# Kernel optimization log

Hardware: AMD Instinct MI355X
Metric: run time of the kernel (lower is better)

The kernel has to match this reference:

```python
import jax, jax.numpy as jnp
import numpy as np

N = 4096      # nodes
IN = 512      # in_features
H = 8         # heads
D = 64        # out_features // heads (out % heads == 0)
EDGE_PROB = 0.01


def setup_inputs() -> dict:
    key = jax.random.key(0)
    kx, ka, kw, ko, kd = jax.random.split(key, 5)
    x = jax.random.normal(kx, (N, IN), dtype=jnp.float32)
    # dense binary adjacency with self-loops (original indexes adj[loc, :] as a mask)
    adj = (jax.random.uniform(ka, (N, N)) < EDGE_PROB).astype(jnp.float32)
    adj = jnp.maximum(adj, jnp.eye(N, dtype=jnp.float32))
    # stacked per-head params (original keeps Python lists of equal-sized heads)
    W = jax.random.normal(kw, (H, IN, D), dtype=jnp.float32) * (1.0 / np.sqrt(IN))
    a_origin = jax.random.normal(ko, (H, D), dtype=jnp.float32) * 0.1
    a_dst = jax.random.normal(kd, (H, D), dtype=jnp.float32) * 0.1
    return {"x": x, "adj": adj, "W": W, "a_origin": a_origin, "a_dst": a_dst}


def reference(x, adj, W, a_origin, a_dst):
    # per-head projection: mx[h] = x @ W[h]  -> [H, N, D]
    mx = jnp.einsum('nf,hfd->hnd', x, W)
    # clacAttn: e_ij = exp(mx_i . a_origin + mx_j . a_dst), masked by adj[i,:], row-normalised
    s_i = jnp.einsum('hnd,hd->hn', mx, a_origin)   # source term (row)
    t_j = jnp.einsum('hnd,hd->hn', mx, a_dst)      # dest term (col)
    logits = s_i[:, :, None] + t_j[:, None, :]     # [H, N, N]
    neg_inf = jnp.finfo(logits.dtype).min
    masked = jnp.where(adj[None] > 0, logits, neg_inf)
    attn = jax.nn.softmax(masked, axis=-1)         # == exp/masked-sum of original
    out_h = jnp.einsum('hij,hjd->hid', attn, mx)   # [H, N, D]
    # hstack over heads -> [N, H*D]
    return jnp.transpose(out_h, (1, 0, 2)).reshape(N, H * D)
```

## Files before the change

### kernel.cpp

```cpp
#include <hip/hip_runtime.h>
#include <hip/hip_bf16.h>

#define N_NODES 4096
#define IN_F    512
#define HEADS   8
#define DH      64
#define HD      512

typedef __bf16 bf16x8 __attribute__((ext_vector_type(8)));
typedef float  f32x4  __attribute__((ext_vector_type(4)));

__device__ __forceinline__ float bf_lo(unsigned u) { return __uint_as_float(u << 16); }
__device__ __forceinline__ float bf_hi(unsigned u) { return __uint_as_float(u & 0xffff0000u); }

#define MAXNBR 512
#define JCAP   128
__global__ __launch_bounds__(256) void k2_scan(const float* __restrict__ adj,
                                               int* __restrict__ deg,
                                               int* __restrict__ jl) {
    __shared__ int jlist[MAXNBR];
    __shared__ int cnt;
    int tid = threadIdx.x;
    int i   = blockIdx.x;
    int lane = tid & 63;
    if (tid == 0) cnt = 0;

    const uint4* arow = (const uint4*)(adj + (size_t)i * N_NODES);
    uint4 v0 = arow[tid];
    uint4 v1 = arow[256 + tid];
    uint4 v2 = arow[512 + tid];
    uint4 v3 = arow[768 + tid];
    int n = (v0.x != 0) + (v0.y != 0) + (v0.z != 0) + (v0.w != 0)
          + (v1.x != 0) + (v1.y != 0) + (v1.z != 0) + (v1.w != 0)
          + (v2.x != 0) + (v2.y != 0) + (v2.z != 0) + (v2.w != 0)
          + (v3.x != 0) + (v3.y != 0) + (v3.z != 0) + (v3.w != 0);
    __syncthreads();

    int pre = n;
    #pragma unroll
    for (int dlt = 1; dlt < 64; dlt <<= 1) {
        int t = __shfl_up(pre, dlt, 64);
        if (lane >= dlt) pre += t;
    }
    int wtot = __shfl(pre, 63, 64);
    int base = 0;
    if (lane == 63) base = atomicAdd(&cnt, wtot);
    base = __shfl(base, 63, 64);
    if (base + wtot <= MAXNBR) {
        int p_ = base + pre - n;
        int jb = tid * 4;
        if (v0.x) jlist[p_++] = jb;
        if (v0.y) jlist[p_++] = jb + 1;
        if (v0.z) jlist[p_++] = jb + 2;
        if (v0.w) jlist[p_++] = jb + 3;
        jb += 1024;
        if (v1.x) jlist[p_++] = jb;
        if (v1.y) jlist[p_++] = jb + 1;
        if (v1.z) jlist[p_++] = jb + 2;
        if (v1.w) jlist[p_++] = jb + 3;
        jb += 1024;
        if (v2.x) jlist[p_++] = jb;
        if (v2.y) jlist[p_++] = jb + 1;
        if (v2.z) jlist[p_++] = jb + 2;
        if (v2.w) jlist[p_++] = jb + 3;
        jb += 1024;
        if (v3.x) jlist[p_++] = jb;
        if (v3.y) jlist[p_++] = jb + 1;
        if (v3.z) jlist[p_++] = jb + 2;
        if (v3.w) jlist[p_++] = jb + 3;
    }
    __syncthreads();
    int c = cnt;
    if (c > JCAP) c = JCAP;
    for (int t = tid; t < c; t += 256) jl[(size_t)i * JCAP + t] = jlist[t];
    if (tid == 0) deg[i] = c;
}

#define KP 72

__global__ __launch_bounds__(256, 2) void k1_gemm(const float* __restrict__ X,
                                                  const float* __restrict__ W,
                                                  const float* __restrict__ a_dst,
                                                  __bf16* __restrict__ C,
                                                  float* __restrict__ et) {
    __shared__ __bf16 As[2][64][KP];
    __shared__ __bf16 Bs[2][64][KP];
    __shared__ float  ts[2][64];
    int tid  = threadIdx.x;
    int h    = blockIdx.x & 7;
    int y    = blockIdx.x >> 3;
    int row0 = y * 64, col0 = h * 64;
    int wave = tid >> 6, lane = tid & 63;
    int wm = wave >> 1, wn = wave & 1;
    int lr = lane & 15, kg = lane >> 4;

    f32x4 acc[2][2] = {};

    int sr = tid >> 3, sc = (tid & 7) * 8;
    const float* aptr0 = X + (size_t)(row0 + sr) * IN_F + sc;
    const float* aptr1 = aptr0 + (size_t)32 * IN_F;
    int dcol = tid & 63, fq = (tid >> 6) * 16;
    const float* wptr = W + ((size_t)h * IN_F + fq) * DH + dcol;

    f32x4 pa00 = *(const f32x4*)aptr0, pa01 = *(const f32x4*)(aptr0 + 4);
    f32x4 pa10 = *(const f32x4*)aptr1, pa11 = *(const f32x4*)(aptr1 + 4);
    float wv[16];
    #pragma unroll
    for (int i = 0; i < 16; ++i) wv[i] = wptr[(size_t)i * DH];

    float ad0 = a_dst[h * DH + wn * 32 + lr];
    float ad1 = a_dst[h * DH + wn * 32 + 16 + lr];

    #pragma unroll
    for (int k = 0; k < IN_F / 64; ++k) {
        int cur = k & 1;
        bf16x8 a0 = { (__bf16)pa00[0], (__bf16)pa00[1], (__bf16)pa00[2], (__bf16)pa00[3],
                      (__bf16)pa01[0], (__bf16)pa01[1], (__bf16)pa01[2], (__bf16)pa01[3] };
        bf16x8 a1 = { (__bf16)pa10[0], (__bf16)pa10[1], (__bf16)pa10[2], (__bf16)pa10[3],
                      (__bf16)pa11[0], (__bf16)pa11[1], (__bf16)pa11[2], (__bf16)pa11[3] };
        bf16x8 b0 = { (__bf16)wv[0],  (__bf16)wv[1],  (__bf16)wv[2],  (__bf16)wv[3],
                      (__bf16)wv[4],  (__bf16)wv[5],  (__bf16)wv[6],  (__bf16)wv[7] };
        bf16x8 b1 = { (__bf16)wv[8],  (__bf16)wv[9],  (__bf16)wv[10], (__bf16)wv[11],
                      (__bf16)wv[12], (__bf16)wv[13], (__bf16)wv[14], (__bf16)wv[15] };
        *(bf16x8*)&As[cur][sr][sc]        = a0;
        *(bf16x8*)&As[cur][sr + 32][sc]   = a1;
        *(bf16x8*)&Bs[cur][dcol][fq]      = b0;
        *(bf16x8*)&Bs[cur][dcol][fq + 8]  = b1;
        if (k + 1 < IN_F / 64) {
            int off = (k + 1) * 64;
            pa00 = *(const f32x4*)(aptr0 + off); pa01 = *(const f32x4*)(aptr0 + off + 4);
            pa10 = *(const f32x4*)(aptr1 + off); pa11 = *(const f32x4*)(aptr1 + off + 4);
            const float* wp = wptr + (size_t)off * DH;
            #pragma unroll
            for (int i = 0; i < 16; ++i) wv[i] = wp[(size_t)i * DH];
        }
        __syncthreads();
        #pragma unroll
        for (int kc = 0; kc < 2; ++kc) {
            bf16x8 af0 = *(const bf16x8*)&As[cur][wm * 32 + lr]     [kc * 32 + kg * 8];
            bf16x8 af1 = *(const bf16x8*)&As[cur][wm * 32 + 16 + lr][kc * 32 + kg * 8];
            bf16x8 bf0 = *(const bf16x8*)&Bs[cur][wn * 32 + lr]     [kc * 32 + kg * 8];
            bf16x8 bf1 = *(const bf16x8*)&Bs[cur][wn * 32 + 16 + lr][kc * 32 + kg * 8];
            acc[0][0] = __builtin_amdgcn_mfma_f32_16x16x32_bf16(af0, bf0, acc[0][0], 0, 0, 0);
            acc[0][1] = __builtin_amdgcn_mfma_f32_16x16x32_bf16(af0, bf1, acc[0][1], 0, 0, 0);
            acc[1][0] = __builtin_amdgcn_mfma_f32_16x16x32_bf16(af1, bf0, acc[1][0], 0, 0, 0);
            acc[1][1] = __builtin_amdgcn_mfma_f32_16x16x32_bf16(af1, bf1, acc[1][1], 0, 0, 0);
        }
    }

    #pragma unroll
    for (int mt = 0; mt < 2; ++mt) {
        #pragma unroll
        for (int nt = 0; nt < 2; ++nt) {
            int col = col0 + wn * 32 + nt * 16 + lr;
            #pragma unroll
            for (int r = 0; r < 4; ++r) {
                int row = row0 + wm * 32 + mt * 16 + kg * 4 + r;
                C[(size_t)row * HD + col] = (__bf16)acc[mt][nt][r];
            }
        }
    }
    #pragma unroll
    for (int mt = 0; mt < 2; ++mt) {
        #pragma unroll
        for (int r = 0; r < 4; ++r) {
            float p = ad0 * acc[mt][0][r] + ad1 * acc[mt][1][r];
            p += __shfl_xor(p, 1);
            p += __shfl_xor(p, 2);
            p += __shfl_xor(p, 4);
            p += __shfl_xor(p, 8);
            if (lr == 0) ts[wn][wm * 32 + mt * 16 + kg * 4 + r] = p;
        }
    }
    __syncthreads();
    if (tid < 64) {
        float t = ts[0][tid] + ts[1][tid];
        et[(size_t)(row0 + tid) * HEADS + h] = __expf(t);
    }
}

__global__ __launch_bounds__(256) void k3_gather(const int* __restrict__ deg,
                                                 const int* __restrict__ jl,
                                                 const __bf16* __restrict__ mx,
                                                 const float* __restrict__ et,
                                                 float* __restrict__ out) {
    __shared__ int   jlist[JCAP];
    __shared__ float red[3][64][9];
    int tid  = threadIdx.x;
    int i    = blockIdx.x;
    int w    = tid >> 6, lane = tid & 63;

    int c = deg[i];
    if (tid < c) jlist[tid] = jl[(size_t)i * JCAP + tid];
    __syncthreads();

    int h = lane >> 3;
    const uint4* mxv = (const uint4*)mx;
    const float* etp = et + h;
    float accA[8] = {0.f,0.f,0.f,0.f,0.f,0.f,0.f,0.f};
    float accB[8] = {0.f,0.f,0.f,0.f,0.f,0.f,0.f,0.f};
    float dA = 0.f, dB = 0.f;

    int  k  = w * 2;
    bool m0 = (k < c), m1 = (k + 1 < c);
    float ea = 0.f, eb = 0.f;
    uint4 va = {0u,0u,0u,0u}, vb = {0u,0u,0u,0u};
    if (m0) { int j = jlist[k];     ea = etp[j * HEADS]; va = mxv[(size_t)j * 64 + lane]; }
    if (m1) { int j = jlist[k + 1]; eb = etp[j * HEADS]; vb = mxv[(size_t)j * 64 + lane]; }

    while (m0) {
        int  kn = k + 8;
        bool n0 = (kn < c), n1 = (kn + 1 < c);
        float ena = 0.f, enb = 0.f;
        uint4 vna = {0u,0u,0u,0u}, vnb = {0u,0u,0u,0u};
        if (n0) { int j = jlist[kn];     ena = etp[j * HEADS]; vna = mxv[(size_t)j * 64 + lane]; }
        if (n1) { int j = jlist[kn + 1]; enb = etp[j * HEADS]; vnb = mxv[(size_t)j * 64 + lane]; }
        accA[0] += ea * bf_lo(va.x);  accA[1] += ea * bf_hi(va.x);
        accA[2] += ea * bf_lo(va.y);  accA[3] += ea * bf_hi(va.y);
        accA[4] += ea * bf_lo(va.z);  accA[5] += ea * bf_hi(va.z);
        accA[6] += ea * bf_lo(va.w);  accA[7] += ea * bf_hi(va.w);
        dA += ea;
        accB[0] += eb * bf_lo(vb.x);  accB[1] += eb * bf_hi(vb.x);
        accB[2] += eb * bf_lo(vb.y);  accB[3] += eb * bf_hi(vb.y);
        accB[4] += eb * bf_lo(vb.z);  accB[5] += eb * bf_hi(vb.z);
        accB[6] += eb * bf_lo(vb.w);  accB[7] += eb * bf_hi(vb.w);
        dB += eb;
        k = kn; m0 = n0; m1 = n1;
        ea = ena; eb = enb; va = vna; vb = vnb;
    }

    float acc[8];
    #pragma unroll
    for (int q = 0; q < 8; ++q) acc[q] = accA[q] + accB[q];
    float d = dA + dB;

    if (w > 0) {
        #pragma unroll
        for (int q = 0; q < 8; ++q) red[w - 1][lane][q] = acc[q];
        red[w - 1][lane][8] = d;
    }
    __syncthreads();
    if (w == 0) {
        #pragma unroll
        for (int g = 0; g < 3; ++g) {
            #pragma unroll
            for (int q = 0; q < 8; ++q) acc[q] += red[g][lane][q];
            d += red[g][lane][8];
        }
        float inv = 1.f / d;
        f32x4 o0 = { acc[0] * inv, acc[1] * inv, acc[2] * inv, acc[3] * inv };
        f32x4 o1 = { acc[4] * inv, acc[5] * inv, acc[6] * inv, acc[7] * inv };
        float* orow = out + (size_t)i * HD + lane * 8;
        *(f32x4*)orow       = o0;
        *(f32x4*)(orow + 4) = o1;
    }
}

extern "C" void kernel_launch(void* const* d_in, const int* in_sizes, int n_in,
                              void* d_out, int out_size, void* d_ws, size_t ws_size,
                              hipStream_t stream) {
    const float* x     = (const float*)d_in[0];
    const float* adj   = (const float*)d_in[1];
    const float* W     = (const float*)d_in[2];
    const float* a_dst = (const float*)d_in[4];
    float* out = (float*)d_out;

    char* ws = (char*)d_ws;
    __bf16* mx  = (__bf16*)ws;
    float*  et  = (float*)(ws + 4194304);
    int*    deg = (int*)  (ws + 4325376);
    int*    jl  = (int*)  (ws + 4341760);

    k2_scan  <<<dim3(N_NODES), dim3(256), 0, stream>>>(adj, deg, jl);
    k1_gemm  <<<dim3(512),     dim3(256), 0, stream>>>(x, W, a_dst, mx, et);
    k3_gather<<<dim3(N_NODES), dim3(256), 0, stream>>>(deg, jl, mx, et, out);
}
```

Baseline: 131.9 us.

## Merge GEMM and adjacency scan into one launch; split gather by head halves

```diff
diff --git a/kernel.cpp b/kernel.cpp
--- a/kernel.cpp
+++ b/kernel.cpp
@@ -15,242 +15,235 @@
 
 #define MAXNBR 512
 #define JCAP   128
-__global__ __launch_bounds__(256) void k2_scan(const float* __restrict__ adj,
-                                               int* __restrict__ deg,
-                                               int* __restrict__ jl) {
-    __shared__ int jlist[MAXNBR];
-    __shared__ int cnt;
-    int tid = threadIdx.x;
-    int i   = blockIdx.x;
-    int lane = tid & 63;
-    if (tid == 0) cnt = 0;
-
-    const uint4* arow = (const uint4*)(adj + (size_t)i * N_NODES);
-    uint4 v0 = arow[tid];
-    uint4 v1 = arow[256 + tid];
-    uint4 v2 = arow[512 + tid];
-    uint4 v3 = arow[768 + tid];
-    int n = (v0.x != 0) + (v0.y != 0) + (v0.z != 0) + (v0.w != 0)
-          + (v1.x != 0) + (v1.y != 0) + (v1.z != 0) + (v1.w != 0)
-          + (v2.x != 0) + (v2.y != 0) + (v2.z != 0) + (v2.w != 0)
-          + (v3.x != 0) + (v3.y != 0) + (v3.z != 0) + (v3.w != 0);
-    __syncthreads();
-
-    int pre = n;
-    #pragma unroll
-    for (int dlt = 1; dlt < 64; dlt <<= 1) {
-        int t = __shfl_up(pre, dlt, 64);
-        if (lane >= dlt) pre += t;
-    }
-    int wtot = __shfl(pre, 63, 64);
-    int base = 0;
-    if (lane == 63) base = atomicAdd(&cnt, wtot);
-    base = __shfl(base, 63, 64);
-    if (base + wtot <= MAXNBR) {
-        int p_ = base + pre - n;
-        int jb = tid * 4;
-        if (v0.x) jlist[p_++] = jb;
-        if (v0.y) jlist[p_++] = jb + 1;
-        if (v0.z) jlist[p_++] = jb + 2;
-        if (v0.w) jlist[p_++] = jb + 3;
-        jb += 1024;
-        if (v1.x) jlist[p_++] = jb;
-        if (v1.y) jlist[p_++] = jb + 1;
-        if (v1.z) jlist[p_++] = jb + 2;
-        if (v1.w) jlist[p_++] = jb + 3;
-        jb += 1024;
-        if (v2.x) jlist[p_++] = jb;
-        if (v2.y) jlist[p_++] = jb + 1;
-        if (v2.z) jlist[p_++] = jb + 2;
-        if (v2.w) jlist[p_++] = jb + 3;
-        jb += 1024;
-        if (v3.x) jlist[p_++] = jb;
-        if (v3.y) jlist[p_++] = jb + 1;
-        if (v3.z) jlist[p_++] = jb + 2;
-        if (v3.w) jlist[p_++] = jb + 3;
-    }
-    __syncthreads();
-    int c = cnt;
-    if (c > JCAP) c = JCAP;
-    for (int t = tid; t < c; t += 256) jl[(size_t)i * JCAP + t] = jlist[t];
-    if (tid == 0) deg[i] = c;
-}
-
-#define KP 72
-
-__global__ __launch_bounds__(256, 2) void k1_gemm(const float* __restrict__ X,
-                                                  const float* __restrict__ W,
-                                                  const float* __restrict__ a_dst,
-                                                  __bf16* __restrict__ C,
-                                                  float* __restrict__ et) {
+#define KP     72
+
+__global__ __launch_bounds__(256, 2) void kA_gemm_scan(
+        const float* __restrict__ X, const float* __restrict__ W,
+        const float* __restrict__ a_dst, const float* __restrict__ adj,
+        __bf16* __restrict__ C, float* __restrict__ et,
+        int* __restrict__ deg, int* __restrict__ jl) {
     __shared__ __bf16 As[2][64][KP];
     __shared__ __bf16 Bs[2][64][KP];
     __shared__ float  ts[2][64];
-    int tid  = threadIdx.x;
-    int h    = blockIdx.x & 7;
-    int y    = blockIdx.x >> 3;
-    int row0 = y * 64, col0 = h * 64;
-    int wave = tid >> 6, lane = tid & 63;
-    int wm = wave >> 1, wn = wave & 1;
-    int lr = lane & 15, kg = lane >> 4;
-
-    f32x4 acc[2][2] = {};
-
-    int sr = tid >> 3, sc = (tid & 7) * 8;
-    const float* aptr0 = X + (size_t)(row0 + sr) * IN_F + sc;
-    const float* aptr1 = aptr0 + (size_t)32 * IN_F;
-    int dcol = tid & 63, fq = (tid >> 6) * 16;
-    const float* wptr = W + ((size_t)h * IN_F + fq) * DH + dcol;
-
-    f32x4 pa00 = *(const f32x4*)aptr0, pa01 = *(const f32x4*)(aptr0 + 4);
-    f32x4 pa10 = *(const f32x4*)aptr1, pa11 = *(const f32x4*)(aptr1 + 4);
-    float wv[16];
-    #pragma unroll
-    for (int i = 0; i < 16; ++i) wv[i] = wptr[(size_t)i * DH];
-
-    float ad0 = a_dst[h * DH + wn * 32 + lr];
-    float ad1 = a_dst[h * DH + wn * 32 + 16 + lr];
-
-    #pragma unroll
-    for (int k = 0; k < IN_F / 64; ++k) {
-        int cur = k & 1;
-        bf16x8 a0 = { (__bf16)pa00[0], (__bf16)pa00[1], (__bf16)pa00[2], (__bf16)pa00[3],
-                      (__bf16)pa01[0], (__bf16)pa01[1], (__bf16)pa01[2], (__bf16)pa01[3] };
-        bf16x8 a1 = { (__bf16)pa10[0], (__bf16)pa10[1], (__bf16)pa10[2], (__bf16)pa10[3],
-                      (__bf16)pa11[0], (__bf16)pa11[1], (__bf16)pa11[2], (__bf16)pa11[3] };
-        bf16x8 b0 = { (__bf16)wv[0],  (__bf16)wv[1],  (__bf16)wv[2],  (__bf16)wv[3],
-                      (__bf16)wv[4],  (__bf16)wv[5],  (__bf16)wv[6],  (__bf16)wv[7] };
-        bf16x8 b1 = { (__bf16)wv[8],  (__bf16)wv[9],  (__bf16)wv[10], (__bf16)wv[11],
-                      (__bf16)wv[12], (__bf16)wv[13], (__bf16)wv[14], (__bf16)wv[15] };
-        *(bf16x8*)&As[cur][sr][sc]        = a0;
-        *(bf16x8*)&As[cur][sr + 32][sc]   = a1;
-        *(bf16x8*)&Bs[cur][dcol][fq]      = b0;
-        *(bf16x8*)&Bs[cur][dcol][fq + 8]  = b1;
-        if (k + 1 < IN_F / 64) {
-            int off = (k + 1) * 64;
-            pa00 = *(const f32x4*)(aptr0 + off); pa01 = *(const f32x4*)(aptr0 + off + 4);
-            pa10 = *(const f32x4*)(aptr1 + off); pa11 = *(const f32x4*)(aptr1 + off + 4);
-            const float* wp = wptr + (size_t)off * DH;
-            #pragma unroll
-            for (int i = 0; i < 16; ++i) wv[i] = wp[(size_t)i * DH];
+    __shared__ int    jlist[MAXNBR];
+    __shared__ int    cnt;
+    int tid = threadIdx.x;
+    int bid = blockIdx.x;
+
+    if (bid < 512) {
+        int h    = bid & 7;
+        int y    = bid >> 3;
+        int row0 = y * 64, col0 = h * 64;
+        int wave = tid >> 6, lane = tid & 63;
+        int wm = wave >> 1, wn = wave & 1;
+        int lr = lane & 15, kg = lane >> 4;
+
+        f32x4 acc[2][2] = {};
+
+        int sr = tid >> 3, sc = (tid & 7) * 8;
+        const float* aptr0 = X + (size_t)(row0 + sr) * IN_F + sc;
+        const float* aptr1 = aptr0 + (size_t)32 * IN_F;
+        int dcol = tid & 63, fq = (tid >> 6) * 16;
+        const float* wptr = W + ((size_t)h * IN_F + fq) * DH + dcol;
+
+        f32x4 pa00 = *(const f32x4*)aptr0, pa01 = *(const f32x4*)(aptr0 + 4);
+        f32x4 pa10 = *(const f32x4*)aptr1, pa11 = *(const f32x4*)(aptr1 + 4);
+        float wv[16];
+        #pragma unroll
+        for (int i = 0; i < 16; ++i) wv[i] = wptr[(size_t)i * DH];
+
+        float ad0 = a_dst[h * DH + wn * 32 + lr];
+        float ad1 = a_dst[h * DH + wn * 32 + 16 + lr];
+
+        #pragma unroll
+        for (int k = 0; k < IN_F / 64; ++k) {
+            int cur = k & 1;
+            bf16x8 a0 = { (__bf16)pa00[0], (__bf16)pa00[1], (__bf16)pa00[2], (__bf16)pa00[3],
+                          (__bf16)pa01[0], (__bf16)pa01[1], (__bf16)pa01[2], (__bf16)pa01[3] };
+            bf16x8 a1 = { (__bf16)pa10[0], (__bf16)pa10[1], (__bf16)pa10[2], (__bf16)pa10[3],
+                          (__bf16)pa11[0], (__bf16)pa11[1], (__bf16)pa11[2], (__bf16)pa11[3] };
+            bf16x8 b0 = { (__bf16)wv[0],  (__bf16)wv[1],  (__bf16)wv[2],  (__bf16)wv[3],
+                          (__bf16)wv[4],  (__bf16)wv[5],  (__bf16)wv[6],  (__bf16)wv[7] };
+            bf16x8 b1 = { (__bf16)wv[8],  (__bf16)wv[9],  (__bf16)wv[10], (__bf16)wv[11],
+                          (__bf16)wv[12], (__bf16)wv[13], (__bf16)wv[14], (__bf16)wv[15] };
+            *(bf16x8*)&As[cur][sr][sc]        = a0;
+            *(bf16x8*)&As[cur][sr + 32][sc]   = a1;
+            *(bf16x8*)&Bs[cur][dcol][fq]      = b0;
+            *(bf16x8*)&Bs[cur][dcol][fq + 8]  = b1;
+            if (k + 1 < IN_F / 64) {
+                int off = (k + 1) * 64;
+                pa00 = *(const f32x4*)(aptr0 + off); pa01 = *(const f32x4*)(aptr0 + off + 4);
+                pa10 = *(const f32x4*)(aptr1 + off); pa11 = *(const f32x4*)(aptr1 + off + 4);
+                const float* wp = wptr + (size_t)off * DH;
+                #pragma unroll
+                for (int i = 0; i < 16; ++i) wv[i] = wp[(size_t)i * DH];
+            }
+            __syncthreads();
+            #pragma unroll
+            for (int kc = 0; kc < 2; ++kc) {
+                bf16x8 af0 = *(const bf16x8*)&As[cur][wm * 32 + lr]     [kc * 32 + kg * 8];
+                bf16x8 af1 = *(const bf16x8*)&As[cur][wm * 32 + 16 + lr][kc * 32 + kg * 8];
+                bf16x8 bf0 = *(const bf16x8*)&Bs[cur][wn * 32 + lr]     [kc * 32 + kg * 8];
+                bf16x8 bf1 = *(const bf16x8*)&Bs[cur][wn * 32 + 16 + lr][kc * 32 + kg * 8];
+                acc[0][0] = __builtin_amdgcn_mfma_f32_16x16x32_bf16(af0, bf0, acc[0][0], 0, 0, 0);
+                acc[0][1] = __builtin_amdgcn_mfma_f32_16x16x32_bf16(af0, bf1, acc[0][1], 0, 0, 0);
+                acc[1][0] = __builtin_amdgcn_mfma_f32_16x16x32_bf16(af1, bf0, acc[1][0], 0, 0, 0);
+                acc[1][1] = __builtin_amdgcn_mfma_f32_16x16x32_bf16(af1, bf1, acc[1][1], 0, 0, 0);
+            }
+        }
+
+        #pragma unroll
+        for (int mt = 0; mt < 2; ++mt) {
+            #pragma unroll
+            for (int nt = 0; nt < 2; ++nt) {
+                int col = col0 + wn * 32 + nt * 16 + lr;
+                #pragma unroll
+                for (int r = 0; r < 4; ++r) {
+                    int row = row0 + wm * 32 + mt * 16 + kg * 4 + r;
+                    C[(size_t)row * HD + col] = (__bf16)acc[mt][nt][r];
+                }
+            }
+        }
+        #pragma unroll
+        for (int mt = 0; mt < 2; ++mt) {
+            #pragma unroll
+            for (int r = 0; r < 4; ++r) {
+                float p = ad0 * acc[mt][0][r] + ad1 * acc[mt][1][r];
+                p += __shfl_xor(p, 1);
+                p += __shfl_xor(p, 2);
+                p += __shfl_xor(p, 4);
+                p += __shfl_xor(p, 8);
+                if (lr == 0) ts[wn][wm * 32 + mt * 16 + kg * 4 + r] = p;
+            }
         }
         __syncthreads();
-        #pragma unroll
-        for (int kc = 0; kc < 2; ++kc) {
-            bf16x8 af0 = *(const bf16x8*)&As[cur][wm * 32 + lr]     [kc * 32 + kg * 8];
-            bf16x8 af1 = *(const bf16x8*)&As[cur][wm * 32 + 16 + lr][kc * 32 + kg * 8];
-            bf16x8 bf0 = *(const bf16x8*)&Bs[cur][wn * 32 + lr]     [kc * 32 + kg * 8];
-            bf16x8 bf1 = *(const bf16x8*)&Bs[cur][wn * 32 + 16 + lr][kc * 32 + kg * 8];
-            acc[0][0] = __builtin_amdgcn_mfma_f32_16x16x32_bf16(af0, bf0, acc[0][0], 0, 0, 0);
-            acc[0][1] = __builtin_amdgcn_mfma_f32_16x16x32_bf16(af0, bf1, acc[0][1], 0, 0, 0);
-            acc[1][0] = __builtin_amdgcn_mfma_f32_16x16x32_bf16(af1, bf0, acc[1][0], 0, 0, 0);
-            acc[1][1] = __builtin_amdgcn_mfma_f32_16x16x32_bf16(af1, bf1, acc[1][1], 0, 0, 0);
-        }
-    }
-
-    #pragma unroll
-    for (int mt = 0; mt < 2; ++mt) {
-        #pragma unroll
-        for (int nt = 0; nt < 2; ++nt) {
-            int col = col0 + wn * 32 + nt * 16 + lr;
-            #pragma unroll
-            for (int r = 0; r < 4; ++r) {
-                int row = row0 + wm * 32 + mt * 16 + kg * 4 + r;
-                C[(size_t)row * HD + col] = (__bf16)acc[mt][nt][r];
-            }
-        }
-    }
-    #pragma unroll
-    for (int mt = 0; mt < 2; ++mt) {
-        #pragma unroll
-        for (int r = 0; r < 4; ++r) {
-            float p = ad0 * acc[mt][0][r] + ad1 * acc[mt][1][r];
-            p += __shfl_xor(p, 1);
-            p += __shfl_xor(p, 2);
-            p += __shfl_xor(p, 4);
-            p += __shfl_xor(p, 8);
-            if (lr == 0) ts[wn][wm * 32 + mt * 16 + kg * 4 + r] = p;
-        }
-    }
-    __syncthreads();
-    if (tid < 64) {
-        float t = ts[0][tid] + ts[1][tid];
-        et[(size_t)(row0 + tid) * HEADS + h] = __expf(t);
+        if (tid < 64) {
+            float t = ts[0][tid] + ts[1][tid];
+            et[(size_t)(row0 + tid) * HEADS + h] = __expf(t);
+        }
+    } else {
+        int i    = bid - 512;
+        int lane = tid & 63;
+        if (tid == 0) cnt = 0;
+
+        const uint4* arow = (const uint4*)(adj + (size_t)i * N_NODES);
+        uint4 v0 = arow[tid];
+        uint4 v1 = arow[256 + tid];
+        uint4 v2 = arow[512 + tid];
+        uint4 v3 = arow[768 + tid];
+        int n = (v0.x != 0) + (v0.y != 0) + (v0.z != 0) + (v0.w != 0)
+              + (v1.x != 0) + (v1.y != 0) + (v1.z != 0) + (v1.w != 0)
+              + (v2.x != 0) + (v2.y != 0) + (v2.z != 0) + (v2.w != 0)
+              + (v3.x != 0) + (v3.y != 0) + (v3.z != 0) + (v3.w != 0);
+        __syncthreads();
+
+        int pre = n;
+        #pragma unroll
+        for (int dlt = 1; dlt < 64; dlt <<= 1) {
+            int t = __shfl_up(pre, dlt, 64);
+            if (lane >= dlt) pre += t;
+        }
+        int wtot = __shfl(pre, 63, 64);
+        int base = 0;
+        if (lane == 63) base = atomicAdd(&cnt, wtot);
+        base = __shfl(base, 63, 64);
+        if (base + wtot <= MAXNBR) {
+            int p_ = base + pre - n;
+            int jb = tid * 4;
+            if (v0.x) jlist[p_++] = jb;
+            if (v0.y) jlist[p_++] = jb + 1;
+            if (v0.z) jlist[p_++] = jb + 2;
+            if (v0.w) jlist[p_++] = jb + 3;
+            jb += 1024;
+            if (v1.x) jlist[p_++] = jb;
+            if (v1.y) jlist[p_++] = jb + 1;
+            if (v1.z) jlist[p_++] = jb + 2;
+            if (v1.w) jlist[p_++] = jb + 3;
+            jb += 1024;
+            if (v2.x) jlist[p_++] = jb;
+            if (v2.y) jlist[p_++] = jb + 1;
+            if (v2.z) jlist[p_++] = jb + 2;
+            if (v2.w) jlist[p_++] = jb + 3;
+            jb += 1024;
+            if (v3.x) jlist[p_++] = jb;
+            if (v3.y) jlist[p_++] = jb + 1;
+            if (v3.z) jlist[p_++] = jb + 2;
+            if (v3.w) jlist[p_++] = jb + 3;
+        }
+        __syncthreads();
+        int c = cnt;
+        if (c > JCAP) c = JCAP;
+        for (int t = tid; t < c; t += 256) jl[(size_t)i * JCAP + t] = jlist[t];
+        if (tid == 0) deg[i] = c;
     }
 }
 
-__global__ __launch_bounds__(256) void k3_gather(const int* __restrict__ deg,
+__global__ __launch_bounds__(256) void kB_gather(const int* __restrict__ deg,
                                                  const int* __restrict__ jl,
                                                  const __bf16* __restrict__ mx,
                                                  const float* __restrict__ et,
                                                  float* __restrict__ out) {
     __shared__ int   jlist[JCAP];
-    __shared__ float red[3][64][9];
-    int tid  = threadIdx.x;
-    int i    = blockIdx.x;
-    int w    = tid >> 6, lane = tid & 63;
+    __shared__ float red[3][32][9];
+    int tid = threadIdx.x;
+    int bid = blockIdx.x;
+    int s   = bid & 1;
+    int i   = bid >> 1;
+    int w   = tid >> 6, lane = tid & 63;
+    int g   = lane >> 5, l5 = lane & 31;
 
     int c = deg[i];
     if (tid < c) jlist[tid] = jl[(size_t)i * JCAP + tid];
     __syncthreads();
 
-    int h = lane >> 3;
-    const uint4* mxv = (const uint4*)mx;
+    int h = s * 4 + (l5 >> 3);
+    const uint4* mxv = (const uint4*)mx + s * 32 + l5;
     const float* etp = et + h;
-    float accA[8] = {0.f,0.f,0.f,0.f,0.f,0.f,0.f,0.f};
-    float accB[8] = {0.f,0.f,0.f,0.f,0.f,0.f,0.f,0.f};
-    float dA = 0.f, dB = 0.f;
-
-    int  k  = w * 2;
-    bool m0 = (k < c), m1 = (k + 1 < c);
-    float ea = 0.f, eb = 0.f;
-    uint4 va = {0u,0u,0u,0u}, vb = {0u,0u,0u,0u};
-    if (m0) { int j = jlist[k];     ea = etp[j * HEADS]; va = mxv[(size_t)j * 64 + lane]; }
-    if (m1) { int j = jlist[k + 1]; eb = etp[j * HEADS]; vb = mxv[(size_t)j * 64 + lane]; }
+
+    float acc[8] = {0.f,0.f,0.f,0.f,0.f,0.f,0.f,0.f};
+    float d = 0.f;
+
+    int  k  = w * 2 + g;
+    bool m0 = (k < c);
+    float e = 0.f;
+    uint4 v = {0u,0u,0u,0u};
+    if (m0) { int j = jlist[k]; e = etp[j * HEADS]; v = mxv[(size_t)j * 64]; }
 
     while (m0) {
         int  kn = k + 8;
-        bool n0 = (kn < c), n1 = (kn + 1 < c);
-        float ena = 0.f, enb = 0.f;
-        uint4 vna = {0u,0u,0u,0u}, vnb = {0u,0u,0u,0u};
-        if (n0) { int j = jlist[kn];     ena = etp[j * HEADS]; vna = mxv[(size_t)j * 64 + lane]; }
-        if (n1) { int j = jlist[kn + 1]; enb = etp[j * HEADS]; vnb = mxv[(size_t)j * 64 + lane]; }
-        accA[0] += ea * bf_lo(va.x);  accA[1] += ea * bf_hi(va.x);
-        accA[2] += ea * bf_lo(va.y);  accA[3] += ea * bf_hi(va.y);
-        accA[4] += ea * bf_lo(va.z);  accA[5] += ea * bf_hi(va.z);
-        accA[6] += ea * bf_lo(va.w);  accA[7] += ea * bf_hi(va.w);
-        dA += ea;
-        accB[0] += eb * bf_lo(vb.x);  accB[1] += eb * bf_hi(vb.x);
-        accB[2] += eb * bf_lo(vb.y);  accB[3] += eb * bf_hi(vb.y);
-        accB[4] += eb * bf_lo(vb.z);  accB[5] += eb * bf_hi(vb.z);
-        accB[6] += eb * bf_lo(vb.w);  accB[7] += eb * bf_hi(vb.w);
-        dB += eb;
-        k = kn; m0 = n0; m1 = n1;
-        ea = ena; eb = enb; va = vna; vb = vnb;
-    }
-
-    float acc[8];
+        bool n0 = (kn < c);
+        float en = 0.f;
+        uint4 vn = {0u,0u,0u,0u};
+        if (n0) { int j = jlist[kn]; en = etp[j * HEADS]; vn = mxv[(size_t)j * 64]; }
+        acc[0] += e * bf_lo(v.x);  acc[1] += e * bf_hi(v.x);
+        acc[2] += e * bf_lo(v.y);  acc[3] += e * bf_hi(v.y);
+        acc[4] += e * bf_lo(v.z);  acc[5] += e * bf_hi(v.z);
+        acc[6] += e * bf_lo(v.w);  acc[7] += e * bf_hi(v.w);
+        d += e;
+        k = kn; m0 = n0; e = en; v = vn;
+    }
+
     #pragma unroll
-    for (int q = 0; q < 8; ++q) acc[q] = accA[q] + accB[q];
-    float d = dA + dB;
-
-    if (w > 0) {
-        #pragma unroll
-        for (int q = 0; q < 8; ++q) red[w - 1][lane][q] = acc[q];
-        red[w - 1][lane][8] = d;
+    for (int q = 0; q < 8; ++q) acc[q] += __shfl_xor(acc[q], 32);
+    d += __shfl_xor(d, 32);
+
+    if (w > 0 && g == 0) {
+        #pragma unroll
+        for (int q = 0; q < 8; ++q) red[w - 1][l5][q] = acc[q];
+        red[w - 1][l5][8] = d;
     }
     __syncthreads();
-    if (w == 0) {
-        #pragma unroll
-        for (int g = 0; g < 3; ++g) {
-            #pragma unroll
-            for (int q = 0; q < 8; ++q) acc[q] += red[g][lane][q];
-            d += red[g][lane][8];
+    if (w == 0 && g == 0) {
+        #pragma unroll
+        for (int r3 = 0; r3 < 3; ++r3) {
+            #pragma unroll
+            for (int q = 0; q < 8; ++q) acc[q] += red[r3][l5][q];
+            d += red[r3][l5][8];
         }
         float inv = 1.f / d;
         f32x4 o0 = { acc[0] * inv, acc[1] * inv, acc[2] * inv, acc[3] * inv };
         f32x4 o1 = { acc[4] * inv, acc[5] * inv, acc[6] * inv, acc[7] * inv };
-        float* orow = out + (size_t)i * HD + lane * 8;
+        float* orow = out + (size_t)i * HD + s * 256 + l5 * 8;
         *(f32x4*)orow       = o0;
         *(f32x4*)(orow + 4) = o1;
     }
@@ -271,7 +264,7 @@
     int*    deg = (int*)  (ws + 4325376);
     int*    jl  = (int*)  (ws + 4341760);
 
-    k2_scan  <<<dim3(N_NODES), dim3(256), 0, stream>>>(adj, deg, jl);
-    k1_gemm  <<<dim3(512),     dim3(256), 0, stream>>>(x, W, a_dst, mx, et);
-    k3_gather<<<dim3(N_NODES), dim3(256), 0, stream>>>(deg, jl, mx, et, out);
+    kA_gemm_scan<<<dim3(512 + N_NODES), dim3(256), 0, stream>>>(x, W, a_dst, adj,
+                                                                mx, et, deg, jl);
+    kB_gather   <<<dim3(N_NODES * 2),   dim3(256), 0, stream>>>(deg, jl, mx, et, out);
 }
```

New measurement: 127.2 us. 1.04x faster.
